# Optimization experiments

Hardware: AMD Instinct MI355X
Metric: run time of the kernel (lower is better)

## Reference

```python
import jax, jax.numpy as jnp
import numpy as np

N = 640   # nodes
H = 64    # hidden_channels == base feature dim (required by MLP input dims)
DEG = 12  # random directed edges per node before symmetrization


def _mlp(x, Wa, ba, Wb, bb):
    # 2-layer MLP: Linear -> ReLU -> Linear (use_bn=False hardcoded in convs; dropout inactive in eval)
    return jax.nn.relu(x @ Wa + ba) @ Wb + bb


def setup_inputs() -> dict:
    key = jax.random.key(0)
    ks = jax.random.split(key, 8)
    x = jax.random.normal(ks[0], (N, H), dtype=jnp.float32)
    E0 = N * DEG
    src = jax.random.randint(ks[1], (E0,), 0, N)
    dst = jax.random.randint(ks[2], (E0,), 0, N)
    # undirected edge list (both directions), matching PyG k_hop_subgraph semantics on symmetric graphs
    edge_index = jnp.stack([jnp.concatenate([src, dst]), jnp.concatenate([dst, src])])
    batch = jnp.zeros((N,), dtype=jnp.int32)  # unused by the module's forward

    def lin(k, fin, fout):
        kw, kb = jax.random.split(k)
        bound = 1.0 / np.sqrt(fin)
        W = jax.random.uniform(kw, (fin, fout), minval=-bound, maxval=bound, dtype=jnp.float32)
        b = jax.random.uniform(kb, (fout,), minval=-bound, maxval=bound, dtype=jnp.float32)
        return W, b

    W1a, b1a = lin(ks[3], H + 2, H)      # convs[1] mlp: (H+t) -> H
    W1b, b1b = lin(ks[4], H, H + 1)      #               H -> (H+t-1)
    W0a, b0a = lin(ks[5], H + 1, H)      # convs[0] mlp: (H+1) -> H
    W0b, b0b = lin(ks[6], H, H)          #               H -> H
    return dict(x=x, W1a=W1a, b1a=b1a, W1b=W1b, b1b=b1b,
                W0a=W0a, b0a=b0a, W0b=W0b, b0b=b0b,
                edge_index=edge_index, batch=batch)


def reference(x, W1a, b1a, W1b, b1b, W0a, b0a, W0b, b0b, edge_index, batch):
    n = x.shape[0]
    # dense adjacency; self-loops have no effect in the original recursion -> zero diagonal
    A = jnp.zeros((n, n), x.dtype).at[edge_index[0], edge_index[1]].set(1.0)
    A = A * (1.0 - jnp.eye(n, dtype=x.dtype))

    # ---- level 1 (last level, r[1]=1), vectorized over all ego pairs (v, u) ----
    # S2(v,u) = nbrs(u) & S_v (common neighbors of v and u, excluding v, u)
    # sum_{w in S2} x_w  and  |S2|
    Y = A[:, :, None] * x[None, :, :]              # [v, w, d]
    T = jnp.einsum('vwd,uw->vud', Y, A)            # [v, u, d] = sum_w A[v,w] A[u,w] x_w
    cnt = A @ A.T                                  # [v, u] common-neighbor counts
    # hv_u = [x_u, 1, 0]; sum over S2 of [x_w, 1, 1]  ->  GIN input [x_u + T, 1 + cnt, cnt]
    inp1 = jnp.concatenate([x[None, :, :] + T,
                            (1.0 + cnt)[..., None],
                            cnt[..., None]], axis=-1)  # [v, u, H+2]
    out1 = _mlp(inp1, W1a, b1a, W1b, b1b)              # [v, u, H+1]

    # ---- level 0 (r[0]=1): GIN over u in S_v ----
    agg = jnp.einsum('vu,vud->vd', A, out1)            # sum of level-1 embeddings over S_v
    hv = jnp.concatenate([x, jnp.zeros((n, 1), x.dtype)], axis=-1)  # [x_v, 0]
    return _mlp(hv + agg, W0a, b0a, W0b, b0b)          # [N, H]
```

## Files before the change

kernel.cpp:

```cpp
#include <hip/hip_runtime.h>

#define NN   640
#define NW   20
#define NWP  24
#define H    64
#define MAXD 96

__global__ __launch_bounds__(512) void prep(
    const int* __restrict__ ei, int E,
    const float* __restrict__ x,
    const float* __restrict__ W1a, const float* __restrict__ W0a,
    const float* __restrict__ W1b, const float* __restrict__ b1b,
    unsigned* __restrict__ bits, float* __restrict__ xa, float* __restrict__ xc,
    float* __restrict__ Wf, float* __restrict__ bf)
{
    const int t = threadIdx.x, lane = t & 63, wave = t >> 6, bid = blockIdx.x;

    if (bid < 320) {
        __shared__ unsigned sb[2 * NW];
        if (t < 2 * NW) sb[t] = 0u;
        __syncthreads();
        for (int k = t; k < E; k += 512) {
            int a = ei[k];
            if ((a >> 1) == bid) {
                int b = ei[k + E];
                if (b != a) atomicOr(&sb[(a & 1) * NW + (b >> 5)], 1u << (b & 31));
            }
        }
        __syncthreads();
        if (t < 2 * NW) bits[(bid * 2 + t / NW) * NWP + (t % NW)] = sb[t];

        if (wave < 4) {
            const int v = bid * 2 + (wave & 1);
            const float* W = (wave < 2) ? W1a : W0a;
            const float xv = x[v * H + lane];
            float a0 = 0, a1 = 0, a2 = 0, a3 = 0;
            #pragma unroll
            for (int k = 0; k < H; k += 4) {
                a0 += __shfl(xv, k, 64)     * W[k * H + lane];
                a1 += __shfl(xv, k + 1, 64) * W[(k + 1) * H + lane];
                a2 += __shfl(xv, k + 2, 64) * W[(k + 2) * H + lane];
                a3 += __shfl(xv, k + 3, 64) * W[(k + 3) * H + lane];
            }
            float r = (a0 + a1) + (a2 + a3);
            if (wave < 2) xa[v * H + lane] = r; else xc[v * H + lane] = r;
        }
    } else if (bid < 328) {
        const int d = (bid - 320) * 8 + wave;
        const float wv = W1b[d * 65 + lane];
        float a0 = 0, a1 = 0, a2 = 0, a3 = 0;
        #pragma unroll
        for (int e = 0; e < 64; e += 4) {
            a0 += __shfl(wv, e, 64)     * W0a[e * H + lane];
            a1 += __shfl(wv, e + 1, 64) * W0a[(e + 1) * H + lane];
            a2 += __shfl(wv, e + 2, 64) * W0a[(e + 2) * H + lane];
            a3 += __shfl(wv, e + 3, 64) * W0a[(e + 3) * H + lane];
        }
        Wf[d * H + lane] = (a0 + a1) + (a2 + a3) + W1b[d * 65 + 64] * W0a[64 * H + lane];
    } else if (wave == 0) {
        const float bv = b1b[lane];
        float a0 = 0, a1 = 0, a2 = 0, a3 = 0;
        #pragma unroll
        for (int e = 0; e < 64; e += 4) {
            a0 += __shfl(bv, e, 64)     * W0a[e * H + lane];
            a1 += __shfl(bv, e + 1, 64) * W0a[(e + 1) * H + lane];
            a2 += __shfl(bv, e + 2, 64) * W0a[(e + 2) * H + lane];
            a3 += __shfl(bv, e + 3, 64) * W0a[(e + 3) * H + lane];
        }
        bf[lane] = (a0 + a1) + (a2 + a3) + b1b[64] * W0a[64 * H + lane];
    }
}

__global__ __launch_bounds__(512) void fused(
    const float* __restrict__ xa,  const float* __restrict__ xc,
    const float* __restrict__ W1a, const float* __restrict__ b1a,
    const float* __restrict__ Wf,  const float* __restrict__ bf,
    const float* __restrict__ b0a,
    const float* __restrict__ W0b, const float* __restrict__ b0b,
    const unsigned* __restrict__ bits,
    float* __restrict__ out)
{
    __shared__ __align__(16) unsigned rowv[NW];
    __shared__ float hpart[8][H];
    __shared__ float hshare[H];
    __shared__ unsigned short ulist[MAXD];
    __shared__ int s_deg;

    const int v = blockIdx.x, t = threadIdx.x;
    const int lane = t & 63, wave = t >> 6;

    if (t < NW) rowv[t] = bits[v * NWP + t];
    __syncthreads();

    if (wave == 0 && lane < NW) {
        int off = 0;
        for (int i = 0; i < lane; ++i) off += __popc(rowv[i]);
        unsigned c = rowv[lane];
        while (c) {
            int b = __ffs(c) - 1; c &= c - 1;
            if (off < MAXD) ulist[off] = (unsigned short)(lane * 32 + b);
            ++off;
        }
        if (lane == NW - 1) s_deg = (off < MAXD) ? off : MAXD;
    }
    __syncthreads();
    const int deg = s_deg;

    const float r64 = W1a[64 * H + lane];
    const float k0  = b1a[lane] + r64;
    const float k1  = r64 + W1a[65 * H + lane];

    const uint4* rv4 = (const uint4*)rowv;
    const uint4 r0 = rv4[0], r1 = rv4[1], r2 = rv4[2], r3 = rv4[3], r4 = rv4[4];

    float hacc = 0.f;
    for (int p = wave; p < deg; p += 8) {
        const int u = ulist[p];
        const uint4* bu = (const uint4*)(bits + u * NWP);
        const uint4 q0 = bu[0], q1 = bu[1], q2 = bu[2], q3 = bu[3], q4 = bu[4];
        unsigned cw[NW] = {
            r0.x & q0.x, r0.y & q0.y, r0.z & q0.z, r0.w & q0.w,
            r1.x & q1.x, r1.y & q1.y, r1.z & q1.z, r1.w & q1.w,
            r2.x & q2.x, r2.y & q2.y, r2.z & q2.z, r2.w & q2.w,
            r3.x & q3.x, r3.y & q3.y, r3.z & q3.z, r3.w & q3.w,
            r4.x & q4.x, r4.y & q4.y, r4.z & q4.z, r4.w & q4.w };
        int cnt = 0;
        #pragma unroll
        for (int j = 0; j < NW; ++j) cnt += __popc(cw[j]);
        float xs = 0.f;
        #pragma unroll
        for (int j = 0; j < NW; ++j) {
            unsigned c = cw[j];
            while (c) {
                int b = __ffs(c) - 1; c &= c - 1;
                xs += xa[(j * 32 + b) * H + lane];
            }
        }
        float h = xa[u * H + lane] + xs + k0 + (float)cnt * k1;
        hacc += fmaxf(h, 0.f);
    }
    hpart[wave][lane] = hacc;
    __syncthreads();

    if (wave == 0) {
        float hs = 0.f;
        #pragma unroll
        for (int w = 0; w < 8; ++w) hs += hpart[w][lane];
        hshare[lane] = hs;
    }
    __syncthreads();
    {
        float s = 0.f;
        #pragma unroll
        for (int i = 0; i < 8; ++i) {
            const int d = wave * 8 + i;
            s += hshare[d] * Wf[d * H + lane];
        }
        hpart[wave][lane] = s;
    }
    __syncthreads();
    if (wave == 0) {
        float s = 0.f;
        #pragma unroll
        for (int w = 0; w < 8; ++w) s += hpart[w][lane];
        float hh = xc[v * H + lane] + (float)deg * bf[lane] + b0a[lane] + s;
        hshare[lane] = fmaxf(hh, 0.f);
    }
    __syncthreads();
    {
        float s = 0.f;
        #pragma unroll
        for (int i = 0; i < 8; ++i) {
            const int d = wave * 8 + i;
            s += hshare[d] * W0b[d * H + lane];
        }
        hpart[wave][lane] = s;
    }
    __syncthreads();
    if (wave == 0) {
        float s = 0.f;
        #pragma unroll
        for (int w = 0; w < 8; ++w) s += hpart[w][lane];
        out[v * H + lane] = b0b[lane] + s;
    }
}

extern "C" void kernel_launch(void* const* d_in, const int* in_sizes, int n_in,
                              void* d_out, int out_size, void* d_ws, size_t ws_size,
                              hipStream_t stream) {
    const float* x   = (const float*)d_in[0];
    const float* W1a = (const float*)d_in[1];
    const float* b1a = (const float*)d_in[2];
    const float* W1b = (const float*)d_in[3];
    const float* b1b = (const float*)d_in[4];
    const float* W0a = (const float*)d_in[5];
    const float* b0a = (const float*)d_in[6];
    const float* W0b = (const float*)d_in[7];
    const float* b0b = (const float*)d_in[8];
    const int*   ei  = (const int*)d_in[9];
    const int    E   = in_sizes[9] / 2;

    char* ws = (char*)d_ws;
    unsigned* bits = (unsigned*)(ws);
    float*    xa   = (float*)(ws + 61440);
    float*    xc   = (float*)(ws + 61440 + 163840);
    float*    Wf   = (float*)(ws + 61440 + 2 * 163840);
    float*    bf   = (float*)(ws + 61440 + 2 * 163840 + 16384);

    prep<<<329, 512, 0, stream>>>(ei, E, x, W1a, W0a, W1b, b1b, bits, xa, xc, Wf, bf);
    fused<<<NN, 512, 0, stream>>>(xa, xc, W1a, b1a, Wf, bf, b0a, W0b, b0b,
                                  bits, (float*)d_out);
}
```

Measured before the change: 24.37 us.

## Fuse prep and main kernels via global atomic grid barrier

Merges the adjacency-building/precompute kernel and the per-node kernel into one launch of 640 blocks of 256 threads, synchronised by a spin-wait grid barrier on a global counter. Bitset construction now uses direct global atomicOr with one edge per thread, instead of each block scanning every edge. A memset clears the bitset and counter first. This removes a kernel launch boundary and the redundant edge scans, but relies on all 640 blocks being co-resident (launch_bounds 256,4) and halves the waves per node for the neighbor loop.

```diff
diff --git a/kernel.cpp b/kernel.cpp
--- a/kernel.cpp
+++ b/kernel.cpp
@@ -6,48 +6,49 @@
 #define H    64
 #define MAXD 96
 
-__global__ __launch_bounds__(512) void prep(
+__global__ __launch_bounds__(256, 4) void rnp_one(
     const int* __restrict__ ei, int E,
     const float* __restrict__ x,
-    const float* __restrict__ W1a, const float* __restrict__ W0a,
+    const float* __restrict__ W1a, const float* __restrict__ b1a,
     const float* __restrict__ W1b, const float* __restrict__ b1b,
-    unsigned* __restrict__ bits, float* __restrict__ xa, float* __restrict__ xc,
-    float* __restrict__ Wf, float* __restrict__ bf)
+    const float* __restrict__ W0a, const float* __restrict__ b0a,
+    const float* __restrict__ W0b, const float* __restrict__ b0b,
+    unsigned* __restrict__ bits, unsigned* __restrict__ ctr,
+    float* __restrict__ xa, float* __restrict__ xc,
+    float* __restrict__ Wf, float* __restrict__ bf,
+    float* __restrict__ out)
 {
-    const int t = threadIdx.x, lane = t & 63, wave = t >> 6, bid = blockIdx.x;
-
-    if (bid < 320) {
-        __shared__ unsigned sb[2 * NW];
-        if (t < 2 * NW) sb[t] = 0u;
-        __syncthreads();
-        for (int k = t; k < E; k += 512) {
-            int a = ei[k];
-            if ((a >> 1) == bid) {
-                int b = ei[k + E];
-                if (b != a) atomicOr(&sb[(a & 1) * NW + (b >> 5)], 1u << (b & 31));
-            }
-        }
-        __syncthreads();
-        if (t < 2 * NW) bits[(bid * 2 + t / NW) * NWP + (t % NW)] = sb[t];
-
-        if (wave < 4) {
-            const int v = bid * 2 + (wave & 1);
-            const float* W = (wave < 2) ? W1a : W0a;
-            const float xv = x[v * H + lane];
-            float a0 = 0, a1 = 0, a2 = 0, a3 = 0;
-            #pragma unroll
-            for (int k = 0; k < H; k += 4) {
-                a0 += __shfl(xv, k, 64)     * W[k * H + lane];
-                a1 += __shfl(xv, k + 1, 64) * W[(k + 1) * H + lane];
-                a2 += __shfl(xv, k + 2, 64) * W[(k + 2) * H + lane];
-                a3 += __shfl(xv, k + 3, 64) * W[(k + 3) * H + lane];
-            }
-            float r = (a0 + a1) + (a2 + a3);
-            if (wave < 2) xa[v * H + lane] = r; else xc[v * H + lane] = r;
-        }
-    } else if (bid < 328) {
-        const int d = (bid - 320) * 8 + wave;
-        const float wv = W1b[d * 65 + lane];
+    __shared__ __align__(16) unsigned rowv[NW];
+    __shared__ float hpart[4][H];
+    __shared__ float hshare[H];
+    __shared__ unsigned short ulist[MAXD];
+    __shared__ int s_deg;
+
+    const int bid = blockIdx.x, t = threadIdx.x;
+    const int lane = t & 63, wave = t >> 6;
+
+    {
+        const int g = bid * 256 + t;
+        if (g < E) {
+            int a = ei[g], b = ei[g + E];
+            if (a != b) atomicOr(&bits[a * NWP + (b >> 5)], 1u << (b & 31));
+        }
+    }
+    if (wave < 2) {
+        const float* W = wave ? W0a : W1a;
+        const float xv = x[bid * H + lane];
+        float a0 = 0, a1 = 0, a2 = 0, a3 = 0;
+        #pragma unroll
+        for (int k = 0; k < H; k += 4) {
+            a0 += __shfl(xv, k, 64)     * W[k * H + lane];
+            a1 += __shfl(xv, k + 1, 64) * W[(k + 1) * H + lane];
+            a2 += __shfl(xv, k + 2, 64) * W[(k + 2) * H + lane];
+            a3 += __shfl(xv, k + 3, 64) * W[(k + 3) * H + lane];
+        }
+        float r = (a0 + a1) + (a2 + a3);
+        if (wave) xc[bid * H + lane] = r; else xa[bid * H + lane] = r;
+    } else if (wave == 2 && bid < 64) {
+        const float wv = W1b[bid * 65 + lane];
         float a0 = 0, a1 = 0, a2 = 0, a3 = 0;
         #pragma unroll
         for (int e = 0; e < 64; e += 4) {
@@ -56,8 +57,9 @@
             a2 += __shfl(wv, e + 2, 64) * W0a[(e + 2) * H + lane];
             a3 += __shfl(wv, e + 3, 64) * W0a[(e + 3) * H + lane];
         }
-        Wf[d * H + lane] = (a0 + a1) + (a2 + a3) + W1b[d * 65 + 64] * W0a[64 * H + lane];
-    } else if (wave == 0) {
+        Wf[bid * H + lane] = (a0 + a1) + (a2 + a3)
+                           + W1b[bid * 65 + 64] * W0a[64 * H + lane];
+    } else if (wave == 3 && bid == 64) {
         const float bv = b1b[lane];
         float a0 = 0, a1 = 0, a2 = 0, a3 = 0;
         #pragma unroll
@@ -69,25 +71,18 @@
         }
         bf[lane] = (a0 + a1) + (a2 + a3) + b1b[64] * W0a[64 * H + lane];
     }
-}
-
-__global__ __launch_bounds__(512) void fused(
-    const float* __restrict__ xa,  const float* __restrict__ xc,
-    const float* __restrict__ W1a, const float* __restrict__ b1a,
-    const float* __restrict__ Wf,  const float* __restrict__ bf,
-    const float* __restrict__ b0a,
-    const float* __restrict__ W0b, const float* __restrict__ b0b,
-    const unsigned* __restrict__ bits,
-    float* __restrict__ out)
-{
-    __shared__ __align__(16) unsigned rowv[NW];
-    __shared__ float hpart[8][H];
-    __shared__ float hshare[H];
-    __shared__ unsigned short ulist[MAXD];
-    __shared__ int s_deg;
-
-    const int v = blockIdx.x, t = threadIdx.x;
-    const int lane = t & 63, wave = t >> 6;
+
+    __syncthreads();
+    if (t == 0) {
+        __threadfence();
+        atomicAdd(ctr, 1u);
+        while (atomicAdd(ctr, 0u) < (unsigned)NN)
+            __builtin_amdgcn_s_sleep(2);
+        __threadfence();
+    }
+    __syncthreads();
+
+    const int v = bid;
 
     if (t < NW) rowv[t] = bits[v * NWP + t];
     __syncthreads();
@@ -114,8 +109,8 @@
     const uint4 r0 = rv4[0], r1 = rv4[1], r2 = rv4[2], r3 = rv4[3], r4 = rv4[4];
 
     float hacc = 0.f;
-    for (int p = wave; p < deg; p += 8) {
-        const int u = ulist[p];
+    for (int p = wave; p < deg; p += 4) {
+        const int u = __builtin_amdgcn_readfirstlane((int)ulist[p]);
         const uint4* bu = (const uint4*)(bits + u * NWP);
         const uint4 q0 = bu[0], q1 = bu[1], q2 = bu[2], q3 = bu[3], q4 = bu[4];
         unsigned cw[NW] = {
@@ -145,15 +140,15 @@
     if (wave == 0) {
         float hs = 0.f;
         #pragma unroll
-        for (int w = 0; w < 8; ++w) hs += hpart[w][lane];
+        for (int w = 0; w < 4; ++w) hs += hpart[w][lane];
         hshare[lane] = hs;
     }
     __syncthreads();
     {
         float s = 0.f;
         #pragma unroll
-        for (int i = 0; i < 8; ++i) {
-            const int d = wave * 8 + i;
+        for (int i = 0; i < 16; ++i) {
+            const int d = wave * 16 + i;
             s += hshare[d] * Wf[d * H + lane];
         }
         hpart[wave][lane] = s;
@@ -162,7 +157,7 @@
     if (wave == 0) {
         float s = 0.f;
         #pragma unroll
-        for (int w = 0; w < 8; ++w) s += hpart[w][lane];
+        for (int w = 0; w < 4; ++w) s += hpart[w][lane];
         float hh = xc[v * H + lane] + (float)deg * bf[lane] + b0a[lane] + s;
         hshare[lane] = fmaxf(hh, 0.f);
     }
@@ -170,8 +165,8 @@
     {
         float s = 0.f;
         #pragma unroll
-        for (int i = 0; i < 8; ++i) {
-            const int d = wave * 8 + i;
+        for (int i = 0; i < 16; ++i) {
+            const int d = wave * 16 + i;
             s += hshare[d] * W0b[d * H + lane];
         }
         hpart[wave][lane] = s;
@@ -180,7 +175,7 @@
     if (wave == 0) {
         float s = 0.f;
         #pragma unroll
-        for (int w = 0; w < 8; ++w) s += hpart[w][lane];
+        for (int w = 0; w < 4; ++w) s += hpart[w][lane];
         out[v * H + lane] = b0b[lane] + s;
     }
 }
@@ -202,12 +197,14 @@
 
     char* ws = (char*)d_ws;
     unsigned* bits = (unsigned*)(ws);
-    float*    xa   = (float*)(ws + 61440);
-    float*    xc   = (float*)(ws + 61440 + 163840);
-    float*    Wf   = (float*)(ws + 61440 + 2 * 163840);
-    float*    bf   = (float*)(ws + 61440 + 2 * 163840 + 16384);
-
-    prep<<<329, 512, 0, stream>>>(ei, E, x, W1a, W0a, W1b, b1b, bits, xa, xc, Wf, bf);
-    fused<<<NN, 512, 0, stream>>>(xa, xc, W1a, b1a, Wf, bf, b0a, W0b, b0b,
-                                  bits, (float*)d_out);
+    unsigned* ctr  = (unsigned*)(ws + 61440);
+    float*    xa   = (float*)(ws + 61504);
+    float*    xc   = (float*)(ws + 61504 + 163840);
+    float*    Wf   = (float*)(ws + 61504 + 2 * 163840);
+    float*    bf   = (float*)(ws + 61504 + 2 * 163840 + 16384);
+
+    hipMemsetAsync(ws, 0, 61504, stream);
+    rnp_one<<<NN, 256, 0, stream>>>(ei, E, x, W1a, b1a, W1b, b1b,
+                                    W0a, b0a, W0b, b0b,
+                                    bits, ctr, xa, xc, Wf, bf, (float*)d_out);
 }
```

Result: slower. 78.46 us (+221.9%).

## Stage neighbor features in LDS and remove serial MLP epilogue syncs

Applied to the files above, without the earlier changes.

Gathers the xa rows of all neighbors of v into shared memory once. The common-neighbor sum then indexes LDS through a prefix-popcount position instead of reading scattered global rows. It also swaps the serial per-lane popcount prefix for a wave shuffle scan and computes the MLP epilogue redundantly in every wave with shuffles, which drops two barriers. It adds about 24KB of LDS per block, a popc per accumulated neighbor, and a 6-waves occupancy hint that may limit registers.

```diff
diff --git a/kernel.cpp b/kernel.cpp
--- a/kernel.cpp
+++ b/kernel.cpp
@@ -71,7 +71,7 @@
     }
 }
 
-__global__ __launch_bounds__(512) void fused(
+__global__ __launch_bounds__(512, 6) void fused(
     const float* __restrict__ xa,  const float* __restrict__ xc,
     const float* __restrict__ W1a, const float* __restrict__ b1a,
     const float* __restrict__ Wf,  const float* __restrict__ bf,
@@ -81,9 +81,11 @@
     float* __restrict__ out)
 {
     __shared__ __align__(16) unsigned rowv[NW];
-    __shared__ float hpart[8][H];
-    __shared__ float hshare[H];
+    __shared__ float xr[MAXD][H];
+    __shared__ float p1[8][H];
+    __shared__ float p2[8][H];
     __shared__ unsigned short ulist[MAXD];
+    __shared__ int pre[NW];
     __shared__ int s_deg;
 
     const int v = blockIdx.x, t = threadIdx.x;
@@ -92,38 +94,49 @@
     if (t < NW) rowv[t] = bits[v * NWP + t];
     __syncthreads();
 
-    if (wave == 0 && lane < NW) {
-        int off = 0;
-        for (int i = 0; i < lane; ++i) off += __popc(rowv[i]);
-        unsigned c = rowv[lane];
+    if (wave == 0) {
+        unsigned word = (lane < NW) ? rowv[lane] : 0u;
+        int pc = __popc(word), scan = pc;
+        #pragma unroll
+        for (int off = 1; off < 32; off <<= 1) {
+            int nb = __shfl_up(scan, off, 64);
+            if (lane >= off) scan += nb;
+        }
+        int o = scan - pc;
+        if (lane < NW) pre[lane] = o;
+        unsigned c = word;
         while (c) {
             int b = __ffs(c) - 1; c &= c - 1;
-            if (off < MAXD) ulist[off] = (unsigned short)(lane * 32 + b);
-            ++off;
-        }
-        if (lane == NW - 1) s_deg = (off < MAXD) ? off : MAXD;
+            if (o < MAXD) ulist[o] = (unsigned short)(lane * 32 + b);
+            ++o;
+        }
+        if (lane == NW - 1) s_deg = (o < MAXD) ? o : MAXD;
     }
     __syncthreads();
     const int deg = s_deg;
+
+    for (int p = wave; p < deg; p += 8)
+        xr[p][lane] = xa[ulist[p] * H + lane];
 
     const float r64 = W1a[64 * H + lane];
     const float k0  = b1a[lane] + r64;
     const float k1  = r64 + W1a[65 * H + lane];
 
-    const uint4* rv4 = (const uint4*)rowv;
-    const uint4 r0 = rv4[0], r1 = rv4[1], r2 = rv4[2], r3 = rv4[3], r4 = rv4[4];
+    unsigned rw[NW];
+    #pragma unroll
+    for (int j = 0; j < NW; ++j) rw[j] = rowv[j];
+    __syncthreads();
 
     float hacc = 0.f;
     for (int p = wave; p < deg; p += 8) {
-        const int u = ulist[p];
-        const uint4* bu = (const uint4*)(bits + u * NWP);
+        const uint4* bu = (const uint4*)(bits + ulist[p] * NWP);
         const uint4 q0 = bu[0], q1 = bu[1], q2 = bu[2], q3 = bu[3], q4 = bu[4];
         unsigned cw[NW] = {
-            r0.x & q0.x, r0.y & q0.y, r0.z & q0.z, r0.w & q0.w,
-            r1.x & q1.x, r1.y & q1.y, r1.z & q1.z, r1.w & q1.w,
-            r2.x & q2.x, r2.y & q2.y, r2.z & q2.z, r2.w & q2.w,
-            r3.x & q3.x, r3.y & q3.y, r3.z & q3.z, r3.w & q3.w,
-            r4.x & q4.x, r4.y & q4.y, r4.z & q4.z, r4.w & q4.w };
+            rw[0]  & q0.x, rw[1]  & q0.y, rw[2]  & q0.z, rw[3]  & q0.w,
+            rw[4]  & q1.x, rw[5]  & q1.y, rw[6]  & q1.z, rw[7]  & q1.w,
+            rw[8]  & q2.x, rw[9]  & q2.y, rw[10] & q2.z, rw[11] & q2.w,
+            rw[12] & q3.x, rw[13] & q3.y, rw[14] & q3.z, rw[15] & q3.w,
+            rw[16] & q4.x, rw[17] & q4.y, rw[18] & q4.z, rw[19] & q4.w };
         int cnt = 0;
         #pragma unroll
         for (int j = 0; j < NW; ++j) cnt += __popc(cw[j]);
@@ -133,55 +146,46 @@
             unsigned c = cw[j];
             while (c) {
                 int b = __ffs(c) - 1; c &= c - 1;
-                xs += xa[(j * 32 + b) * H + lane];
+                int pos = pre[j] + __popc(rw[j] & ((1u << b) - 1));
+                xs += xr[pos][lane];
             }
         }
-        float h = xa[u * H + lane] + xs + k0 + (float)cnt * k1;
+        float h = xr[p][lane] + xs + k0 + (float)cnt * k1;
         hacc += fmaxf(h, 0.f);
     }
-    hpart[wave][lane] = hacc;
-    __syncthreads();
-
+    p1[wave][lane] = hacc;
+    __syncthreads();
+
+    float hs = 0.f;
+    #pragma unroll
+    for (int w = 0; w < 8; ++w) hs += p1[w][lane];
+    float s = 0.f;
+    #pragma unroll
+    for (int i = 0; i < 8; ++i) {
+        const int d = wave * 8 + i;
+        s += __shfl(hs, d, 64) * Wf[d * H + lane];
+    }
+    p2[wave][lane] = s;
+    __syncthreads();
+
+    float s2 = 0.f;
+    #pragma unroll
+    for (int w = 0; w < 8; ++w) s2 += p2[w][lane];
+    const float hh = fmaxf(xc[v * H + lane] + (float)deg * bf[lane]
+                           + b0a[lane] + s2, 0.f);
+    float o = 0.f;
+    #pragma unroll
+    for (int i = 0; i < 8; ++i) {
+        const int d = wave * 8 + i;
+        o += __shfl(hh, d, 64) * W0b[d * H + lane];
+    }
+    p1[wave][lane] = o;
+    __syncthreads();
     if (wave == 0) {
-        float hs = 0.f;
-        #pragma unroll
-        for (int w = 0; w < 8; ++w) hs += hpart[w][lane];
-        hshare[lane] = hs;
-    }
-    __syncthreads();
-    {
-        float s = 0.f;
-        #pragma unroll
-        for (int i = 0; i < 8; ++i) {
-            const int d = wave * 8 + i;
-            s += hshare[d] * Wf[d * H + lane];
-        }
-        hpart[wave][lane] = s;
-    }
-    __syncthreads();
-    if (wave == 0) {
-        float s = 0.f;
-        #pragma unroll
-        for (int w = 0; w < 8; ++w) s += hpart[w][lane];
-        float hh = xc[v * H + lane] + (float)deg * bf[lane] + b0a[lane] + s;
-        hshare[lane] = fmaxf(hh, 0.f);
-    }
-    __syncthreads();
-    {
-        float s = 0.f;
-        #pragma unroll
-        for (int i = 0; i < 8; ++i) {
-            const int d = wave * 8 + i;
-            s += hshare[d] * W0b[d * H + lane];
-        }
-        hpart[wave][lane] = s;
-    }
-    __syncthreads();
-    if (wave == 0) {
-        float s = 0.f;
-        #pragma unroll
-        for (int w = 0; w < 8; ++w) s += hpart[w][lane];
-        out[v * H + lane] = b0b[lane] + s;
+        float oo = b0b[lane];
+        #pragma unroll
+        for (int w = 0; w < 8; ++w) oo += p1[w][lane];
+        out[v * H + lane] = oo;
     }
 }
 
```

Result: no change. 24.54 us (+0.7%).
